# Optimization experiments

Measured on AMD Instinct MI355X. Metric: run time of the kernel, lower is better.

The kernel has to match this reference:

```python
import jax, jax.numpy as jnp
import numpy as np
from jax import lax

# pywt db5 analysis filter bank (frozen buffers in the torch module)
DEC_LO = np.array([0.003335725285001549, -0.012580751999015526, -0.006241490213011705,
                   0.07757149384006515, -0.03224486958502952, -0.24229488706619015,
                   0.13842814590110342, 0.7243085284385744, 0.6038292697974729,
                   0.160102397974125], dtype=np.float32)
DEC_HI = np.array([-0.160102397974125, 0.6038292697974729, -0.7243085284385744,
                   0.13842814590110342, 0.24229488706619015, -0.03224486958502952,
                   -0.07757149384006515, -0.006241490213011705, 0.012580751999015526,
                   0.003335725285001549], dtype=np.float32)
NUM_LEVELS = 8  # min(round(log2(131072)), max_level=8)


def _conv1d(x, w, padding, lhs_dilation=(1,), groups=1):
    # x: [N, C, L], w: [O, I, K]; cross-correlation, matching torch F.conv1d
    return lax.conv_general_dilated(
        x, w, window_strides=(1,), padding=[padding], lhs_dilation=lhs_dilation,
        dimension_numbers=("NCH", "OIH", "NCH"), feature_group_count=groups)


def setup_inputs() -> dict:
    key = jax.random.key(0)
    k1, k2 = jax.random.split(key)
    x = jax.random.normal(k1, (128, 131072), dtype=jnp.float32)
    # small scale keeps the 8-level synthesis cascade numerically tame
    idwt_filters = jax.random.normal(k2, (128, 8, 2, 32), dtype=jnp.float32) * 0.05
    return {"x": x, "idwt_filters": idwt_filters}


def reference(x, idwt_filters):
    # x: [B, T]; idwt_filters: [B, levels, 2, kw] with kw even
    B, T = x.shape
    w_lo = jnp.asarray(DEC_LO).reshape(1, 1, -1)
    w_hi = jnp.asarray(DEC_HI).reshape(1, 1, -1)
    pad = DEC_LO.shape[0] // 2  # 5 -> conv output length L+1 for kernel 10

    # --- analysis DWT (frozen db5 filters), lengths: T/2^l + 1 per band ---
    lo = x[:, None, :]                       # [B,1,T]
    his = []
    for _ in range(NUM_LEVELS):
        y_lo = _conv1d(lo, w_lo, (pad, pad))
        y_hi = _conv1d(lo, w_hi, (pad, pad))
        lo = y_lo[:, :, ::2]
        his.append(y_hi[:, :, ::2])          # [B,1,T/2^l+1]

    # --- synthesis IDWT with predicted per-example filters (groups=B) ---
    kw = idwt_filters.shape[-1]
    p = kw // 2 - 1
    prev = jnp.transpose(lo, (1, 0, 2))      # [1,B,n]: batch as channels
    for i in range(NUM_LEVELS - 1, -1, -1):
        rec_lo = idwt_filters[:, i, 0, :][:, None, :]   # [B,1,kw]
        rec_hi = idwt_filters[:, i, 1, :][:, None, :]
        hi = jnp.transpose(his[i], (1, 0, 2))           # [1,B,n]
        # lhs_dilation=2 == zero-stuffing even indices; asym pad (p, p+1)
        # reproduces torch's trailing zero at index 2n-1; out length = 2n-1
        y_lo = _conv1d(prev, rec_lo, (p, p + 1), lhs_dilation=(2,), groups=B)
        y_hi = _conv1d(hi, rec_hi, (p, p + 1), lhs_dilation=(2,), groups=B)
        prev = y_lo + y_hi
    return prev[0, :, :-1]                   # [B, T]
```

## Files before the change

### kernel.cpp

```cpp
#include <hip/hip_runtime.h>


static __constant__ float c_dec_lo[10] = {
    0.003335725285001549f, -0.012580751999015526f, -0.006241490213011705f,
    0.07757149384006515f, -0.03224486958502952f, -0.24229488706619015f,
    0.13842814590110342f, 0.7243085284385744f, 0.6038292697974729f,
    0.160102397974125f};
static __constant__ float c_dec_hi[10] = {
    -0.160102397974125f, 0.6038292697974729f, -0.7243085284385744f,
    0.13842814590110342f, 0.24229488706619015f, -0.03224486958502952f,
    -0.07757149384006515f, -0.006241490213011705f, 0.012580751999015526f,
    0.003335725285001549f};

__device__ inline float4 ldz4(const float* __restrict__ row, int j, int L) {
  if (j >= 0 && j + 3 < L) return *reinterpret_cast<const float4*>(row + j);
  float4 r;
  r.x = (j + 0 >= 0 && j + 0 < L) ? row[j + 0] : 0.f;
  r.y = (j + 1 >= 0 && j + 1 < L) ? row[j + 1] : 0.f;
  r.z = (j + 2 >= 0 && j + 2 < L) ? row[j + 2] : 0.f;
  r.w = (j + 3 >= 0 && j + 3 < L) ? row[j + 3] : 0.f;
  return r;
}

__device__ inline void load20(const float* src, int base, float* v) {
#pragma unroll
  for (int q = 0; q < 5; ++q) {
    const float4 t = *reinterpret_cast<const float4*>(src + base + 4 * q);
    v[4 * q + 0] = t.x; v[4 * q + 1] = t.y;
    v[4 * q + 2] = t.z; v[4 * q + 3] = t.w;
  }
}

__device__ inline void load20z(const float* __restrict__ src, int base, int L,
                               float* v) {
#pragma unroll
  for (int q = 0; q < 5; ++q) {
    const float4 t = ldz4(src, base + 4 * q, L);
    v[4 * q + 0] = t.x; v[4 * q + 1] = t.y;
    v[4 * q + 2] = t.z; v[4 * q + 3] = t.w;
  }
}

__device__ inline void load12(const float* src, float* v) {
#pragma unroll
  for (int q = 0; q < 3; ++q) {
    const float4 t = *reinterpret_cast<const float4*>(src + 4 * q);
    v[4 * q + 0] = t.x; v[4 * q + 1] = t.y;
    v[4 * q + 2] = t.z; v[4 * q + 3] = t.w;
  }
}

__device__ inline void fir10x2(const float* v, float* lo, float* hv) {
#pragma unroll
  for (int i = 0; i < 4; ++i) {
    float a = 0.f, h = 0.f;
#pragma unroll
    for (int k = 0; k < 10; ++k) {
      const float xx = v[2 * i + 3 + k];
      a += xx * c_dec_lo[k];
      h += xx * c_dec_hi[k];
    }
    lo[i] = a; hv[i] = h;
  }
}

__device__ inline void fir10x2_split(const float* e, const float* o,
                                     float* lo, float* hv) {
#pragma unroll
  for (int i = 0; i < 4; ++i) {
    float a = 0.f, h = 0.f;
#pragma unroll
    for (int m = 0; m < 5; ++m) {
      const float ov = o[i + 1 + m], ev = e[i + 2 + m];
      a += ov * c_dec_lo[2 * m] + ev * c_dec_lo[2 * m + 1];
      h += ov * c_dec_hi[2 * m] + ev * c_dec_hi[2 * m + 1];
    }
    lo[i] = a; hv[i] = h;
  }
}

__device__ inline void store_hi(float* hg, int A, int idx, const float* hv,
                                int es, int ee) {
  if (idx >= es && idx + 3 < ee) {
    *reinterpret_cast<float4*>(hg + A + idx) =
        make_float4(hv[0], hv[1], hv[2], hv[3]);
  } else {
#pragma unroll
    for (int i = 0; i < 4; ++i)
      if (idx + i >= es && idx + i < ee) hg[A + idx + i] = hv[i];
  }
}

__device__ inline void st4(float* dst, const float* a) {
  *reinterpret_cast<float4*>(dst) = make_float4(a[0], a[1], a[2], a[3]);
}

__device__ inline void store_pad_split(float* E, float* O, int idx,
                                       const float* lo, int vlo, int vhi) {
#pragma unroll
  for (int i = 0; i < 4; ++i) {
    const int s = idx + i;
    const float val = (s >= vlo && s < vhi) ? lo[i] : 0.f;
    if (s & 1) O[s >> 1] = val;
    else E[s >> 1] = val;
  }
}

__device__ inline void wave_sync() {
  __builtin_amdgcn_wave_barrier();
  asm volatile("s_waitcnt lgkmcnt(0)" ::: "memory");
  __builtin_amdgcn_wave_barrier();
}

template <bool FAST>
__device__ inline void wl_level0(const float* __restrict__ xr, float* E0,
                                 float* O0, float* __restrict__ h0, int A0,
                                 int xoff, int vlo, int vhi, int eeh,
                                 int lane) {
#pragma unroll
  for (int i = 0; i < 5; ++i) {
    const int idx = 4 * lane + 256 * i;
    if (idx < 1108) {
      float v[20];
      if (FAST) load20(xr, 2 * idx + xoff, v);
      else load20z(xr, 2 * idx + xoff, 131072, v);
      float lo[4], hv[4];
      fir10x2(v, lo, hv);
      if (FAST) {
        const int j = idx >> 1;
        *reinterpret_cast<float2*>(E0 + j) = make_float2(lo[0], lo[2]);
        *reinterpret_cast<float2*>(O0 + j) = make_float2(lo[1], lo[3]);
        if (idx >= 56 && idx < 1080) st4(h0 + A0 + idx, hv);
      } else {
        store_pad_split(E0, O0, idx, lo, vlo, vhi);
        store_hi(h0, A0, idx, hv, 56, eeh);
      }
    }
  }
}

template <bool FAST>
__device__ inline void wl_levelN(const float* Ein, const float* Oin,
                                 float* Eout, float* Oout,
                                 float* __restrict__ hg, int A, int NOUT,
                                 int iters, int esHi, int eeHiF, int vlo,
                                 int vhi, int lane) {
  for (int i = 0; i < iters; ++i) {
    const int idx = 4 * lane + 256 * i;
    if (idx < NOUT) {
      float e[12], o[12];
      load12(Ein + idx, e);
      load12(Oin + idx, o);
      float lo[4], hv[4];
      fir10x2_split(e, o, lo, hv);
      if (FAST) {
        const int j = idx >> 1;
        *reinterpret_cast<float2*>(Eout + j) = make_float2(lo[0], lo[2]);
        *reinterpret_cast<float2*>(Oout + j) = make_float2(lo[1], lo[3]);
        if (idx >= esHi && idx < eeHiF) st4(hg + A + idx, hv);
      } else {
        store_pad_split(Eout, Oout, idx, lo, vlo, vhi);
        store_hi(hg, A, idx, hv, esHi, min(eeHiF, vhi));
      }
    }
  }
}

template <bool FAST>
__device__ inline void wl_level3(const float* Ein, const float* Oin,
                                 float* __restrict__ l3,
                                 float* __restrict__ h3, int T, int ne3,
                                 int lane) {
  const int idx = 4 * lane;
  if (idx >= 128) return;
  float e[12], o[12];
  load12(Ein + idx, e);
  load12(Oin + idx, o);
  float lo[4], hv[4];
  fir10x2_split(e, o, lo, hv);
  if (FAST) {
    st4(l3 + T + idx, lo);
    st4(h3 + T + idx, hv);
  } else {
    store_hi(l3, T, idx, lo, 0, ne3);
    store_hi(h3, T, idx, hv, 0, ne3);
  }
}

__global__ __launch_bounds__(256) void fwd03(
    const float* __restrict__ x, float* __restrict__ hi0,
    float* __restrict__ hi1, float* __restrict__ hi2,
    float* __restrict__ hi3, float* __restrict__ lo3) {
  const int b = blockIdx.y;
  const int widx = threadIdx.x >> 6;
  const int lane = threadIdx.x & 63;
  const int gw = blockIdx.x * 4 + widx;
  __shared__ float W[7744];
  float* E0 = W + widx * 1936;
  float* O0 = E0 + 556;
  float* E1 = O0 + 556;
  float* O1 = E1 + 276;
  float* E2 = O1 + 276;
  float* O2 = E2 + 136;
  if (gw > 64) return;
  const int T = gw * 128;
  const float* xr = x + (size_t)b * 131072;
  float* h0 = hi0 + (size_t)b * 65540;
  float* h1 = hi1 + (size_t)b * 32772;
  float* h2 = hi2 + (size_t)b * 16388;
  float* h3 = hi3 + (size_t)b * 8196;
  float* l3 = lo3 + (size_t)b * 8196;
  const int A0 = 8 * T - 56, A1 = 4 * T - 24, A2 = 2 * T - 8;
  const int xoff = 16 * T - 120;

  if (gw >= 1 && gw <= 62) {
    wl_level0<true>(xr, E0, O0, h0, A0, xoff, 0, 0, 0, lane);
    wave_sync();
    wl_levelN<true>(E0, O0, E1, O1, h1, A1, 548, 3, 24, 536, 0, 0, lane);
    wave_sync();
    wl_levelN<true>(E1, O1, E2, O2, h2, A2, 268, 2, 8, 264, 0, 0, lane);
    wave_sync();
    wl_level3<true>(E2, O2, l3, h3, T, 128, lane);
  } else {
    wl_level0<false>(xr, E0, O0, h0, A0, xoff, (A0 < 0) ? -A0 : 0,
                     min(1108, 65537 - A0), min(1080, 65537 - A0), lane);
    wave_sync();
    wl_levelN<false>(E0, O0, E1, O1, h1, A1, 548, 3, 24, 536,
                     (A1 < 0) ? -A1 : 0, min(548, 32769 - A1), lane);
    wave_sync();
    wl_levelN<false>(E1, O1, E2, O2, h2, A2, 268, 2, 8, 264,
                     (A2 < 0) ? -A2 : 0, min(268, 16385 - A2), lane);
    wave_sync();
    wl_level3<false>(E2, O2, l3, h3, T, min(128, 8193 - T), lane);
  }
}

__device__ inline void inv_accum(const float* p, const float* h,
                                 const float4* wpk, float* acc) {
#pragma unroll
  for (int i = 0; i < 8; ++i) acc[i] = 0.f;
#pragma unroll
  for (int m = 0; m < 16; ++m) {
    const float4 w = wpk[m];
#pragma unroll
    for (int e = 0; e < 4; ++e) {
      const float pe = p[e + 1 + m], he = h[e + 1 + m];
      acc[2 * e + 0] += pe * w.y + he * w.w;
      acc[2 * e + 1] += pe * w.x + he * w.z;
    }
  }
}

__global__ __launch_bounds__(256) void inv_big(
    const float* __restrict__ prev, const float* __restrict__ hicoef,
    const float* __restrict__ filt, int level, int L, int sIn, int Tout,
    int sOut, float* __restrict__ out) {
  const int c = blockIdx.y;
  __shared__ float4 wpack[16];
  const int tid = threadIdx.x;
  if (tid < 16) {
    const float* f = filt + ((size_t)c * 8 + level) * 64;
    wpack[tid] = make_float4(f[2 * tid], f[2 * tid + 1],
                             f[32 + 2 * tid], f[32 + 2 * tid + 1]);
  }
  __syncthreads();
  const int g = blockIdx.x * 256 + tid;
  const int t0 = 16 * g;
  if (t0 >= Tout) return;
  const int U = 8 * g - 8;
  const float* prow = prev + (size_t)c * sIn;
  const float* hrow = hicoef + (size_t)c * sIn;
  float p[24], h[24];
  const bool interior = (U >= 0) && (U + 23 < L) && (t0 + 15 < Tout);
  if (interior) {
#pragma unroll
    for (int q = 0; q < 6; ++q) {
      float4 a = *reinterpret_cast<const float4*>(prow + U + 4 * q);
      p[4 * q + 0] = a.x; p[4 * q + 1] = a.y; p[4 * q + 2] = a.z; p[4 * q + 3] = a.w;
      float4 bb = *reinterpret_cast<const float4*>(hrow + U + 4 * q);
      h[4 * q + 0] = bb.x; h[4 * q + 1] = bb.y; h[4 * q + 2] = bb.z; h[4 * q + 3] = bb.w;
    }
  } else {
#pragma unroll
    for (int q = 0; q < 24; ++q) {
      const int j = U + q;
      p[q] = (j >= 0 && j < L) ? prow[j] : 0.f;
      h[q] = (j >= 0 && j < L) ? hrow[j] : 0.f;
    }
  }
  float acc[16];
#pragma unroll
  for (int i = 0; i < 16; ++i) acc[i] = 0.f;
#pragma unroll
  for (int m = 0; m < 16; ++m) {
    const float4 w = wpack[m];
#pragma unroll
    for (int e = 0; e < 8; ++e) {
      const float pv = p[e + 1 + m], hv = h[e + 1 + m];
      acc[2 * e + 0] += pv * w.y + hv * w.w;
      acc[2 * e + 1] += pv * w.x + hv * w.z;
    }
  }
  float* orow = out + (size_t)c * sOut;
  if (interior) {
#pragma unroll
    for (int q = 0; q < 4; ++q)
      *reinterpret_cast<float4*>(orow + t0 + 4 * q) =
          make_float4(acc[4 * q], acc[4 * q + 1], acc[4 * q + 2], acc[4 * q + 3]);
  } else {
#pragma unroll
    for (int i = 0; i < 16; ++i)
      if (t0 + i < Tout) orow[t0 + i] = acc[i];
  }
}

__device__ inline void fwd_tail_level(const float* __restrict__ in,
                                      float* __restrict__ outp, int L, int D,
                                      float* __restrict__ hirow, int tid) {
  for (int d0 = 4 * tid; d0 < D; d0 += 2048) {
    const int jb = 2 * d0 - 8;
    float v[20];
    const bool interior = (jb >= 0) && (jb + 19 < L) && (d0 + 3 < D);
    if (interior) {
      load20(in, jb, v);
    } else {
#pragma unroll
      for (int q = 0; q < 20; ++q) {
        const int j = jb + q;
        v[q] = (j >= 0 && j < L) ? in[j] : 0.f;
      }
    }
    float lo[4], hv[4];
    fir10x2(v, lo, hv);
    if (interior) {
      st4(outp + d0, lo);
      st4(hirow + d0, hv);
    } else {
#pragma unroll
      for (int i = 0; i < 4; ++i)
        if (d0 + i < D) { outp[d0 + i] = lo[i]; hirow[d0 + i] = hv[i]; }
    }
  }
}

__device__ inline void inv_tail_level(const float* __restrict__ pin,
                                      float* __restrict__ pout, int L,
                                      const float* __restrict__ hirow,
                                      const float* __restrict__ filt, int c,
                                      int level, int tid, float4* wpack) {
  __syncthreads();
  if (tid < 16) {
    const float* f = filt + ((size_t)c * 8 + level) * 64;
    wpack[tid] = make_float4(f[2 * tid], f[2 * tid + 1], f[32 + 2 * tid],
                             f[32 + 2 * tid + 1]);
  }
  __syncthreads();
  const int Tout = 2 * L - 1;
  for (int t0 = 8 * tid; t0 < Tout; t0 += 4096) {
    const int U = t0 / 2 - 8;
    float p[20], h[20];
    if (U >= 0 && U + 19 < L) {
      load20(pin, U, p);
      load20(hirow, U, h);
    } else {
#pragma unroll
      for (int q = 0; q < 20; ++q) {
        const int j = U + q;
        p[q] = (j >= 0 && j < L) ? pin[j] : 0.f;
        h[q] = (j >= 0 && j < L) ? hirow[j] : 0.f;
      }
    }
    float acc[8];
    inv_accum(p, h, wpack, acc);
    if (t0 + 7 < Tout) {
      st4(pout + t0, acc);
      st4(pout + t0 + 4, acc + 4);
    } else {
#pragma unroll
      for (int i = 0; i < 8; ++i)
        if (t0 + i < Tout) pout[t0 + i] = acc[i];
    }
  }
}

__global__ __launch_bounds__(512) void mid_fused(
    const float* __restrict__ lo3, const float* __restrict__ filt,
    float* __restrict__ prev3out) {
  const int b = blockIdx.x;
  __shared__ float A[8200];
  __shared__ float Bb[4104];
  __shared__ float H4[4100];
  __shared__ float H5[2052];
  __shared__ float H6[1028];
  __shared__ float H7[516];
  __shared__ float4 wpack[16];
  const int tid = threadIdx.x;
  const float* row = lo3 + (size_t)b * 8196;
  for (int j4 = tid; j4 < 2048; j4 += 512)
    *reinterpret_cast<float4*>(A + 4 * j4) =
        *reinterpret_cast<const float4*>(row + 4 * j4);
  if (tid == 0) A[8192] = row[8192];
  __syncthreads();
  fwd_tail_level(A, Bb, 8193, 4097, H4, tid);
  __syncthreads();
  fwd_tail_level(Bb, A, 4097, 2049, H5, tid);
  __syncthreads();
  fwd_tail_level(A, Bb, 2049, 1025, H6, tid);
  __syncthreads();
  fwd_tail_level(Bb, A, 1025, 513, H7, tid);
  inv_tail_level(A, Bb, 513, H7, filt, b, 7, tid, wpack);
  inv_tail_level(Bb, A, 1025, H6, filt, b, 6, tid, wpack);
  inv_tail_level(A, Bb, 2049, H5, filt, b, 5, tid, wpack);
  inv_tail_level(Bb, prev3out + (size_t)b * 8196, 4097, H4, filt, b, 4, tid,
                 wpack);
}

extern "C" void kernel_launch(void* const* d_in, const int* in_sizes, int n_in,
                              void* d_out, int out_size, void* d_ws,
                              size_t ws_size, hipStream_t stream) {
  const float* x = (const float*)d_in[0];
  const float* filt = (const float*)d_in[1];
  float* out = (float*)d_out;
  float* ws = (float*)d_ws;

  const int B = 128;
  float* lo3buf = ws;
  float* prev3buf = lo3buf + (size_t)B * 8196;
  float* hi0 = prev3buf + (size_t)B * 8196;
  float* hi1 = hi0 + (size_t)B * 65540;
  float* hi2 = hi1 + (size_t)B * 32772;
  float* hi3 = hi2 + (size_t)B * 16388;
  float* prev2buf = hi3 + (size_t)B * 8196;
  float* prev1buf = prev2buf + (size_t)B * 16388;
  float* prev0buf = prev1buf + (size_t)B * 32772;

  hipLaunchKernelGGL(fwd03, dim3(17, B), dim3(256), 0, stream, x, hi0, hi1,
                     hi2, hi3, lo3buf);
  hipLaunchKernelGGL(mid_fused, dim3(B), dim3(512), 0, stream, lo3buf, filt,
                     prev3buf);

  auto launch_inv = [&](const float* prev, const float* hv, int level, int L,
                        int sIn, int Tout, int sOut, float* dst) {
    const int tpr = (Tout + 15) / 16;
    dim3 grid((tpr + 255) / 256, B);
    hipLaunchKernelGGL(inv_big, grid, dim3(256), 0, stream, prev, hv, filt,
                       level, L, sIn, Tout, sOut, dst);
  };
  launch_inv(prev3buf, hi3, 3, 8193, 8196, 16385, 16388, prev2buf);
  launch_inv(prev2buf, hi2, 2, 16385, 16388, 32769, 32772, prev1buf);
  launch_inv(prev1buf, hi1, 1, 32769, 32772, 65537, 65540, prev0buf);
  launch_inv(prev0buf, hi0, 0, 65537, 65540, 131072, 131072, out);
}
```

Measured before the change: 132.8 us.

## Fuse pairs of inverse synthesis levels into one kernel with recompute

```diff
diff --git a/kernel.cpp b/kernel.cpp
--- a/kernel.cpp
+++ b/kernel.cpp
@@ -235,78 +235,115 @@
   }
 }
 
+template <int NE>
+__device__ inline void accum_pairs(const float* p, const float* h,
+                                   const float4* wpk, float* acc) {
+#pragma unroll
+  for (int i = 0; i < 2 * NE; ++i) acc[i] = 0.f;
+#pragma unroll
+  for (int m = 0; m < 16; ++m) {
+    const float4 w = wpk[m];
+#pragma unroll
+    for (int e = 0; e < NE; ++e) {
+      const float pv = p[e + 1 + m], hv = h[e + 1 + m];
+      acc[2 * e + 0] += pv * w.y + hv * w.w;
+      acc[2 * e + 1] += pv * w.x + hv * w.z;
+    }
+  }
+}
+
 __device__ inline void inv_accum(const float* p, const float* h,
                                  const float4* wpk, float* acc) {
-#pragma unroll
-  for (int i = 0; i < 8; ++i) acc[i] = 0.f;
-#pragma unroll
-  for (int m = 0; m < 16; ++m) {
-    const float4 w = wpk[m];
-#pragma unroll
-    for (int e = 0; e < 4; ++e) {
-      const float pe = p[e + 1 + m], he = h[e + 1 + m];
-      acc[2 * e + 0] += pe * w.y + he * w.w;
-      acc[2 * e + 1] += pe * w.x + he * w.z;
-    }
-  }
-}
-
-__global__ __launch_bounds__(256) void inv_big(
-    const float* __restrict__ prev, const float* __restrict__ hicoef,
-    const float* __restrict__ filt, int level, int L, int sIn, int Tout,
-    int sOut, float* __restrict__ out) {
+  accum_pairs<4>(p, h, wpk, acc);
+}
+
+__global__ __launch_bounds__(256) void inv_fused2(
+    const float* __restrict__ prevU, const float* __restrict__ hiU,
+    const float* __restrict__ hiL, const float* __restrict__ filt, int lvlU,
+    int lvlL, int Lu, int sU, int Lmid, int sL, int Tout, int sOut,
+    float* __restrict__ out) {
   const int c = blockIdx.y;
-  __shared__ float4 wpack[16];
+  __shared__ float4 wp[32];
   const int tid = threadIdx.x;
-  if (tid < 16) {
-    const float* f = filt + ((size_t)c * 8 + level) * 64;
-    wpack[tid] = make_float4(f[2 * tid], f[2 * tid + 1],
-                             f[32 + 2 * tid], f[32 + 2 * tid + 1]);
+  if (tid < 32) {
+    const int lvl = (tid < 16) ? lvlU : lvlL;
+    const int m = tid & 15;
+    const float* f = filt + ((size_t)c * 8 + lvl) * 64;
+    wp[tid] = make_float4(f[2 * m], f[2 * m + 1], f[32 + 2 * m],
+                          f[32 + 2 * m + 1]);
   }
   __syncthreads();
   const int g = blockIdx.x * 256 + tid;
   const int t0 = 16 * g;
   if (t0 >= Tout) return;
-  const int U = 8 * g - 8;
-  const float* prow = prev + (size_t)c * sIn;
-  const float* hrow = hicoef + (size_t)c * sIn;
-  float p[24], h[24];
-  const bool interior = (U >= 0) && (U + 23 < L) && (t0 + 15 < Tout);
+  const int U0 = 8 * g - 8;
+  const int V0 = 4 * g - 12;
+  const float* pu = prevU + (size_t)c * sU;
+  const float* hu = hiU + (size_t)c * sU;
+  const float* hl = hiL + (size_t)c * sL;
+
+  const bool interior = (V0 >= 0) && (V0 + 27 < Lu) && (U0 >= 0) &&
+                        (U0 + 23 < Lmid) && (t0 + 15 < Tout);
+  float pw[28], hw[28];
   if (interior) {
 #pragma unroll
+    for (int q = 0; q < 7; ++q) {
+      const float4 a = *reinterpret_cast<const float4*>(pu + V0 + 4 * q);
+      pw[4 * q + 0] = a.x; pw[4 * q + 1] = a.y;
+      pw[4 * q + 2] = a.z; pw[4 * q + 3] = a.w;
+      const float4 b = *reinterpret_cast<const float4*>(hu + V0 + 4 * q);
+      hw[4 * q + 0] = b.x; hw[4 * q + 1] = b.y;
+      hw[4 * q + 2] = b.z; hw[4 * q + 3] = b.w;
+    }
+  } else {
+#pragma unroll
+    for (int q = 0; q < 7; ++q) {
+      const float4 a = ldz4(pu, V0 + 4 * q, Lu);
+      pw[4 * q + 0] = a.x; pw[4 * q + 1] = a.y;
+      pw[4 * q + 2] = a.z; pw[4 * q + 3] = a.w;
+      const float4 b = ldz4(hu, V0 + 4 * q, Lu);
+      hw[4 * q + 0] = b.x; hw[4 * q + 1] = b.y;
+      hw[4 * q + 2] = b.z; hw[4 * q + 3] = b.w;
+    }
+  }
+
+  float pm[24];
+  accum_pairs<12>(pw, hw, wp, pm);
+  if (!interior) {
+#pragma unroll
+    for (int q = 0; q < 24; ++q) {
+      const int j = U0 + q;
+      if (j < 0 || j >= Lmid) pm[q] = 0.f;
+    }
+  }
+
+  float hm[24];
+  if (interior) {
+#pragma unroll
     for (int q = 0; q < 6; ++q) {
-      float4 a = *reinterpret_cast<const float4*>(prow + U + 4 * q);
-      p[4 * q + 0] = a.x; p[4 * q + 1] = a.y; p[4 * q + 2] = a.z; p[4 * q + 3] = a.w;
-      float4 bb = *reinterpret_cast<const float4*>(hrow + U + 4 * q);
-      h[4 * q + 0] = bb.x; h[4 * q + 1] = bb.y; h[4 * q + 2] = bb.z; h[4 * q + 3] = bb.w;
-    }
-  } else {
-#pragma unroll
-    for (int q = 0; q < 24; ++q) {
-      const int j = U + q;
-      p[q] = (j >= 0 && j < L) ? prow[j] : 0.f;
-      h[q] = (j >= 0 && j < L) ? hrow[j] : 0.f;
-    }
-  }
+      const float4 b = *reinterpret_cast<const float4*>(hl + U0 + 4 * q);
+      hm[4 * q + 0] = b.x; hm[4 * q + 1] = b.y;
+      hm[4 * q + 2] = b.z; hm[4 * q + 3] = b.w;
+    }
+  } else {
+#pragma unroll
+    for (int q = 0; q < 6; ++q) {
+      const float4 b = ldz4(hl, U0 + 4 * q, Lmid);
+      hm[4 * q + 0] = b.x; hm[4 * q + 1] = b.y;
+      hm[4 * q + 2] = b.z; hm[4 * q + 3] = b.w;
+    }
+  }
+
   float acc[16];
-#pragma unroll
-  for (int i = 0; i < 16; ++i) acc[i] = 0.f;
-#pragma unroll
-  for (int m = 0; m < 16; ++m) {
-    const float4 w = wpack[m];
-#pragma unroll
-    for (int e = 0; e < 8; ++e) {
-      const float pv = p[e + 1 + m], hv = h[e + 1 + m];
-      acc[2 * e + 0] += pv * w.y + hv * w.w;
-      acc[2 * e + 1] += pv * w.x + hv * w.z;
-    }
-  }
+  accum_pairs<8>(pm, hm, wp + 16, acc);
+
   float* orow = out + (size_t)c * sOut;
   if (interior) {
 #pragma unroll
     for (int q = 0; q < 4; ++q)
       *reinterpret_cast<float4*>(orow + t0 + 4 * q) =
-          make_float4(acc[4 * q], acc[4 * q + 1], acc[4 * q + 2], acc[4 * q + 3]);
+          make_float4(acc[4 * q], acc[4 * q + 1], acc[4 * q + 2],
+                      acc[4 * q + 3]);
   } else {
 #pragma unroll
     for (int i = 0; i < 16; ++i)
@@ -430,24 +467,17 @@
   float* hi1 = hi0 + (size_t)B * 65540;
   float* hi2 = hi1 + (size_t)B * 32772;
   float* hi3 = hi2 + (size_t)B * 16388;
-  float* prev2buf = hi3 + (size_t)B * 8196;
-  float* prev1buf = prev2buf + (size_t)B * 16388;
-  float* prev0buf = prev1buf + (size_t)B * 32772;
+  float* prev1buf = hi3 + (size_t)B * 8196;
 
   hipLaunchKernelGGL(fwd03, dim3(17, B), dim3(256), 0, stream, x, hi0, hi1,
                      hi2, hi3, lo3buf);
   hipLaunchKernelGGL(mid_fused, dim3(B), dim3(512), 0, stream, lo3buf, filt,
                      prev3buf);
 
-  auto launch_inv = [&](const float* prev, const float* hv, int level, int L,
-                        int sIn, int Tout, int sOut, float* dst) {
-    const int tpr = (Tout + 15) / 16;
-    dim3 grid((tpr + 255) / 256, B);
-    hipLaunchKernelGGL(inv_big, grid, dim3(256), 0, stream, prev, hv, filt,
-                       level, L, sIn, Tout, sOut, dst);
-  };
-  launch_inv(prev3buf, hi3, 3, 8193, 8196, 16385, 16388, prev2buf);
-  launch_inv(prev2buf, hi2, 2, 16385, 16388, 32769, 32772, prev1buf);
-  launch_inv(prev1buf, hi1, 1, 32769, 32772, 65537, 65540, prev0buf);
-  launch_inv(prev0buf, hi0, 0, 65537, 65540, 131072, 131072, out);
-}
+  hipLaunchKernelGGL(inv_fused2, dim3(9, B), dim3(256), 0, stream, prev3buf,
+                     hi3, hi2, filt, 3, 2, 8193, 8196, 16385, 16388, 32769,
+                     32772, prev1buf);
+  hipLaunchKernelGGL(inv_fused2, dim3(32, B), dim3(256), 0, stream, prev1buf,
+                     hi1, hi0, filt, 1, 0, 32769, 32772, 65537, 65540, 131072,
+                     131072, out);
+}
```

New measurement: 156.4 us. 17.8% more time.
